# Optimization experiments

Measured on AMD Instinct MI355X. Metric: run time of the kernel, lower is better.

Reference implementation:

```python
import jax, jax.numpy as jnp
import numpy as np

Q, T, N = 1024, 256, 100
EPS = 1e-6


def setup_inputs() -> dict:
    key = jax.random.key(0)
    ks = jax.random.split(key, 8)
    return {
        'pred_curve_points': jax.random.normal(ks[0], (1, Q, N, 3), jnp.float32),
        'pred_curve_logits': jax.random.normal(ks[1], (1, Q, 2), jnp.float32),
        'pred_curve_type': jax.random.normal(ks[2], (1, Q, 4), jnp.float32),
        'closed_curve_logits': jax.random.normal(ks[3], (1, Q, 2), jnp.float32),
        'tgt_curve_points': jax.random.normal(ks[4], (T, N, 3), jnp.float32),
        'tgt_labels': jax.random.randint(ks[5], (T,), 0, 4, jnp.int64),
        'tgt_is_closed': jax.random.randint(ks[6], (T,), 0, 2, jnp.int64),
        'curve_length_weighting': jax.random.uniform(ks[7], (T,), jnp.float32),
    }


def reference(pred_curve_points, pred_curve_logits, pred_curve_type,
              closed_curve_logits, tgt_curve_points, tgt_labels,
              tgt_is_closed, curve_length_weighting):
    preds = pred_curve_points[0]                       # [Q,N,3] (batch_size=1)
    q, n, _ = preds.shape
    t = tgt_curve_points.shape[0]

    type_prob = jax.nn.softmax(pred_curve_type[0], axis=-1)      # [Q,4]
    valid_prob = jax.nn.softmax(pred_curve_logits[0], axis=-1)   # [Q,2]
    closed_prob = jax.nn.softmax(closed_curve_logits[0], axis=-1)  # [Q,2]

    # classification cost [Q,T]
    cost_class = (-jnp.log(type_prob[:, tgt_labels] + EPS)
                  - jnp.log(valid_prob[:, 0:1] + EPS)
                  - jnp.log(closed_prob[:, tgt_is_closed] + EPS))

    # cyclic variants of each target curve: all rolls of fwd + reversed orders
    j = jnp.arange(n)
    R = (j[None, :] - j[:, None]) % n                  # R[k, j] = (j-k) % n
    v_fwd = tgt_curve_points[:, R, :]                  # [T,N,N,3]
    v_bwd = tgt_curve_points[:, ::-1, :][:, R, :]      # [T,N,N,3]
    variants = jnp.concatenate([v_fwd, v_bwd], axis=1).reshape(t, 2 * n, 3 * n)
    preds_flat = preds.reshape(q, 3 * n)

    # squared cdist on flattened curves / n  (|a|^2 + |b|^2 - 2 a.b)
    ab = jnp.einsum('tvd,qd->tvq', variants, preds_flat)
    v2 = jnp.sum(tgt_curve_points ** 2, axis=(1, 2))[:, None, None]
    p2 = jnp.sum(preds_flat ** 2, axis=1)[None, None, :]
    d2 = jnp.maximum(v2 + p2 - 2.0 * ab, 0.0) / n      # [T,2N,Q]

    # closed curves: min over all 2N cyclic variants, remap reversed ids
    closed_d = d2.min(axis=1)                          # [T,Q]
    closed_ids = jnp.argmin(d2, axis=1)
    closed_ids = jnp.where(closed_ids > n - 1, 2 * n - 1 - closed_ids, closed_ids)
    # open curves: min over identity (variant 0) and full reversal (variant N)
    open_d = jnp.minimum(d2[:, 0], d2[:, n])           # [T,Q]

    is_closed_b = (tgt_is_closed > 0)[:, None]
    geom = jnp.where(is_closed_b, closed_d, open_d).T  # [Q,T]
    ids = jnp.where(is_closed_b, closed_ids, 0).T.astype(jnp.int32)

    geom = geom * curve_length_weighting[None, :]
    C = 1.0 * geom + 1.0 * cost_class                  # cost_position=cost_class=1
    return C, ids
```

## Files before the change

### kernel.cpp

```cpp
#include <hip/hip_runtime.h>
#include <hip/hip_fp16.h>

#define Q_TOT 1024
#define T_TOT 256
#define NPTS  100
#define KD    300
#define EPSV  1e-6f

#define KSTEPS 10
#define EXTOFF 40
#define EXTLEN 672

typedef _Float16 f16;
typedef _Float16 f16x8 __attribute__((ext_vector_type(8)));
typedef float    f32x4 __attribute__((ext_vector_type(4)));
#define MFMA16 __builtin_amdgcn_mfma_f32_16x16x32_f16

#define WS_PF 1280

__global__ __launch_bounds__(256) void prep_all(const float* __restrict__ preds,
                                                const float* __restrict__ tgt,
                                                float* __restrict__ ws)
{
    __shared__ __align__(16) float ext[16][308];
    const int b   = blockIdx.x;
    const int tid = threadIdx.x;

    {
        const float4* src = (const float4*)(preds + b*16*KD);
        for (int i = tid; i < 1200; i += 256) {
            int row = i / 75;
            int c   = i - row*75;
            *(float4*)&ext[row][c*4] = src[i];
        }
    }
    __syncthreads();

    f16x8* pf = (f16x8*)(ws + WS_PF) + b*1280;
    for (int j = tid; j < 1280; j += 256) {
        int lane = j & 63;
        int r    = j >> 6;
        int s    = r & 1;
        int ks   = r >> 1;
        int qr   = lane & 15;
        int kb   = ks*32 + (lane >> 4)*8;
        f16x8 v;
        #pragma unroll
        for (int jj = 0; jj < 8; ++jj) {
            int k = kb + jj;
            float x = (k < KD) ? ext[qr][k] : 0.f;
            f16 h = (f16)x;
            v[jj] = s ? (f16)(x - (float)h) : h;
        }
        pf[j] = v;
    }

    const int wv   = tid >> 6;
    const int lane = tid & 63;
    #pragma unroll
    for (int rr = 0; rr < 4; ++rr) {
        int row = wv*4 + rr;
        float s = 0.f;
        for (int k = lane; k < KD; k += 64) s = fmaf(ext[row][k], ext[row][k], s);
        #pragma unroll
        for (int m = 1; m < 64; m <<= 1) s += __shfl_xor(s, m, 64);
        if (lane == 0) ws[b*16 + row] = s;
    }
    {
        const float* base = tgt + (b*4 + wv)*KD;
        float s = 0.f;
        for (int k = lane; k < KD; k += 64) s = fmaf(base[k], base[k], s);
        #pragma unroll
        for (int m = 1; m < 64; m <<= 1) s += __shfl_xor(s, m, 64);
        if (lane == 0) ws[1024 + b*4 + wv] = s;
    }
}

template<int SEL, int VOFF>
__device__ __forceinline__ void sweep2(const f16 (*sext)[8][EXTLEN],
                                       const f16x8* __restrict__ pfrag,
                                       int ntg0, int lane, int col, int rg, int cA,
                                       float v2t, const float (&p2v)[2],
                                       float (&minD)[2], int (&minI)[2],
                                       float (*sopen)[256], int ntl0)
{
    f32x4 acc[7][2];
    #pragma unroll
    for (int h = 0; h < 7; ++h)
        #pragma unroll
        for (int nt = 0; nt < 2; ++nt) acc[h][nt] = (f32x4){0.f,0.f,0.f,0.f};

    #pragma clang loop unroll(disable)
    for (int ks = 0; ks < KSTEPS; ++ks) {
        f16x8 bh[2], bl[2];
        #pragma unroll
        for (int nt = 0; nt < 2; ++nt) {
            const int fi = ((ntg0+nt)*KSTEPS + ks)*128 + lane;
            bh[nt] = pfrag[fi];
            bl[nt] = pfrag[fi + 64];
        }
        {
            f16x8 ah[7];
            #pragma unroll
            for (int h = 0; h < 7; ++h) {
                const int idx = EXTOFF + 300 - 48*h - 3*col + 8*rg - cA + 32*ks;
                ah[h] = *(const f16x8*)&sext[SEL][cA][idx];
            }
            #pragma unroll
            for (int nt = 0; nt < 2; ++nt)
                #pragma unroll
                for (int h = 0; h < 7; ++h)
                    acc[h][nt] = MFMA16(ah[h], bh[nt], acc[h][nt], 0,0,0);
            #pragma unroll
            for (int nt = 0; nt < 2; ++nt)
                #pragma unroll
                for (int h = 0; h < 7; ++h)
                    acc[h][nt] = MFMA16(ah[h], bl[nt], acc[h][nt], 0,0,0);
        }
        {
            f16x8 alo[7];
            #pragma unroll
            for (int h = 0; h < 7; ++h) {
                const int idx = EXTOFF + 300 - 48*h - 3*col + 8*rg - cA + 32*ks;
                alo[h] = *(const f16x8*)&sext[SEL+1][cA][idx];
            }
            #pragma unroll
            for (int nt = 0; nt < 2; ++nt)
                #pragma unroll
                for (int h = 0; h < 7; ++h)
                    acc[h][nt] = MFMA16(alo[h], bh[nt], acc[h][nt], 0,0,0);
        }
    }

    #pragma unroll
    for (int h = 0; h < 7; ++h) {
        const int ab = h*16 + rg*4;
        #pragma unroll
        for (int nt = 0; nt < 2; ++nt) {
            const float s2 = v2t + p2v[nt];
            #pragma unroll
            for (int r = 0; r < 4; ++r) {
                const int al = ab + r;
                if (al < 100) {
                    float d2 = fmaxf(fmaf(-2.f, acc[h][nt][r], s2), 0.f) * 0.01f;
                    int vlog = VOFF + al;
                    if (d2 < minD[nt]) { minD[nt] = d2; minI[nt] = vlog; }
                    if (al == 0) sopen[VOFF ? 1 : 0][(ntl0+nt)*16 + col] = d2;
                }
            }
        }
    }
}

__global__ __launch_bounds__(512) void matcher_mfma(
    const float* __restrict__ ws,
    const float* __restrict__ tgt,
    const float* __restrict__ plog,
    const float* __restrict__ ptyp,
    const float* __restrict__ clog,
    const int*   __restrict__ labels,
    const int*   __restrict__ iscl,
    const float* __restrict__ clw,
    float* __restrict__ out)
{
    __shared__ __align__(16) f16 sext[4][8][EXTLEN];
    __shared__ float redD[1024];
    __shared__ int   redI[1024];
    __shared__ float sopen[2][256];

    const int t    = blockIdx.x;
    const int nb   = blockIdx.y;
    const int tid  = threadIdx.x;
    const int lane = tid & 63;
    const int w    = tid >> 6;
    const int col  = lane & 15;
    const int rg   = lane >> 4;
    const int ntl0 = w*2;
    const int ntg0 = nb*16 + ntl0;

    const float* tg = tgt + t*KD;
    for (int x = tid; x < EXTLEN; x += 512) {
        int e = x - EXTOFF;
        float vF = 0.f, vR = 0.f;
        if (e >= 0 && e < 600) {
            int m = (e >= 300) ? e - 300 : e;
            vF = tg[m];
            int jj = m / 3, c3 = m - 3*jj;
            vR = tg[(NPTS-1-jj)*3 + c3];
        }
        f16 fh = (f16)vF, fl = (f16)(vF - (float)fh);
        f16 rh = (f16)vR, rl = (f16)(vR - (float)rh);
        #pragma unroll
        for (int c = 0; c < 8; ++c) {
            int y = x - c;
            if (y >= 0) {
                sext[0][c][y] = fh; sext[1][c][y] = fl;
                sext[2][c][y] = rh; sext[3][c][y] = rl;
            }
        }
    }

    const float v2t = ws[1024 + t];
    float p2v[2];
    #pragma unroll
    for (int nt = 0; nt < 2; ++nt) p2v[nt] = ws[(ntg0+nt)*16 + col];
    const f16x8* __restrict__ pfrag = (const f16x8*)(ws + WS_PF);
    const int cA = (EXTOFF + 300 - 3*col) & 7;
    __syncthreads();

    float minD[2]; int minI[2];
    #pragma unroll
    for (int nt = 0; nt < 2; ++nt) { minD[nt] = 3.4028235e38f; minI[nt] = 0; }

    sweep2<0,  0>(sext, pfrag, ntg0, lane, col, rg, cA, v2t, p2v, minD, minI, sopen, ntl0);
    sweep2<2,100>(sext, pfrag, ntg0, lane, col, rg, cA, v2t, p2v, minD, minI, sopen, ntl0);

    #pragma unroll
    for (int nt = 0; nt < 2; ++nt) {
        redD[(ntl0+nt)*64 + lane] = minD[nt];
        redI[(ntl0+nt)*64 + lane] = minI[nt];
    }
    __syncthreads();

    if (tid < 256) {
        const int lq   = tid;
        const int tile = lq >> 4;
        const int cc   = lq & 15;
        const int base = tile*64 + cc;
        float bd = redD[base]; int bi = redI[base];
        #pragma unroll
        for (int g = 1; g < 4; ++g) {
            float d = redD[base + g*16]; int i = redI[base + g*16];
            if (d < bd || (d == bd && i < bi)) { bd = d; bi = i; }
        }
        const int q = nb*256 + lq;
        int mapped = (bi <= NPTS-1) ? bi : (2*NPTS-1 - bi);
        float od   = fminf(sopen[0][lq], sopen[1][lq]);
        int   isc  = iscl[t];
        float geom = isc ? bd : od;
        int   ido  = isc ? mapped : 0;
        geom *= clw[t];

        float t0 = ptyp[q*4+0], t1 = ptyp[q*4+1];
        float t2 = ptyp[q*4+2], t3 = ptyp[q*4+3];
        float mx = fmaxf(fmaxf(t0,t1), fmaxf(t2,t3));
        float e0 = expf(t0-mx), e1 = expf(t1-mx), e2 = expf(t2-mx), e3 = expf(t3-mx);
        float rs = 1.0f/(e0+e1+e2+e3);
        int lab  = labels[t];
        float el = (lab == 0) ? e0 : (lab == 1) ? e1 : (lab == 2) ? e2 : e3;
        float cost = -logf(el*rs + EPSV);
        float v0 = plog[q*2+0], v1 = plog[q*2+1];
        cost += -logf(1.0f/(1.0f + expf(v1-v0)) + EPSV);
        float c0 = clog[q*2+0], c1 = clog[q*2+1];
        float pc = isc ? (1.0f/(1.0f + expf(c0-c1))) : (1.0f/(1.0f + expf(c1-c0)));
        cost += -logf(pc + EPSV);

        float C = geom + cost;
        out[q*T_TOT + t]               = C;
        out[Q_TOT*T_TOT + q*T_TOT + t] = (float)ido;
    }
}

extern "C" void kernel_launch(void* const* d_in, const int* in_sizes, int n_in,
                              void* d_out, int out_size, void* d_ws, size_t ws_size,
                              hipStream_t stream)
{
    const float* preds  = (const float*)d_in[0];
    const float* plog   = (const float*)d_in[1];
    const float* ptyp   = (const float*)d_in[2];
    const float* clog   = (const float*)d_in[3];
    const float* tgt    = (const float*)d_in[4];
    const int*   labels = (const int*)d_in[5];
    const int*   iscl   = (const int*)d_in[6];
    const float* clw    = (const float*)d_in[7];
    float* out = (float*)d_out;
    float* ws  = (float*)d_ws;

    prep_all    <<<dim3(64),       dim3(256), 0, stream>>>(preds, tgt, ws);
    matcher_mfma<<<dim3(T_TOT, 4), dim3(512), 0, stream>>>(
        ws, tgt, plog, ptyp, clog, labels, iscl, clw, out);
}
```

Baseline: 161.8 us.

## Fuse prep kernel into matcher, converting preds to split-f16 fragments inline

Removes the separate prep kernel and its workspace round trip. The matcher now computes target and prediction squared norms itself and builds the hi/lo f16 B fragments directly from fp32 preds inside each k-step. This saves one launch and the global write and read of the fragments. In exchange, every block redoes the conversion and norm work, reading fp32 rows per lane with strided access instead of coalesced pre-packed fragments. The conversion is also done twice, once per sweep.

```diff
diff --git a/kernel.cpp b/kernel.cpp
--- a/kernel.cpp
+++ b/kernel.cpp
@@ -16,70 +16,11 @@
 typedef float    f32x4 __attribute__((ext_vector_type(4)));
 #define MFMA16 __builtin_amdgcn_mfma_f32_16x16x32_f16
 
-#define WS_PF 1280
-
-__global__ __launch_bounds__(256) void prep_all(const float* __restrict__ preds,
-                                                const float* __restrict__ tgt,
-                                                float* __restrict__ ws)
-{
-    __shared__ __align__(16) float ext[16][308];
-    const int b   = blockIdx.x;
-    const int tid = threadIdx.x;
-
-    {
-        const float4* src = (const float4*)(preds + b*16*KD);
-        for (int i = tid; i < 1200; i += 256) {
-            int row = i / 75;
-            int c   = i - row*75;
-            *(float4*)&ext[row][c*4] = src[i];
-        }
-    }
-    __syncthreads();
-
-    f16x8* pf = (f16x8*)(ws + WS_PF) + b*1280;
-    for (int j = tid; j < 1280; j += 256) {
-        int lane = j & 63;
-        int r    = j >> 6;
-        int s    = r & 1;
-        int ks   = r >> 1;
-        int qr   = lane & 15;
-        int kb   = ks*32 + (lane >> 4)*8;
-        f16x8 v;
-        #pragma unroll
-        for (int jj = 0; jj < 8; ++jj) {
-            int k = kb + jj;
-            float x = (k < KD) ? ext[qr][k] : 0.f;
-            f16 h = (f16)x;
-            v[jj] = s ? (f16)(x - (float)h) : h;
-        }
-        pf[j] = v;
-    }
-
-    const int wv   = tid >> 6;
-    const int lane = tid & 63;
-    #pragma unroll
-    for (int rr = 0; rr < 4; ++rr) {
-        int row = wv*4 + rr;
-        float s = 0.f;
-        for (int k = lane; k < KD; k += 64) s = fmaf(ext[row][k], ext[row][k], s);
-        #pragma unroll
-        for (int m = 1; m < 64; m <<= 1) s += __shfl_xor(s, m, 64);
-        if (lane == 0) ws[b*16 + row] = s;
-    }
-    {
-        const float* base = tgt + (b*4 + wv)*KD;
-        float s = 0.f;
-        for (int k = lane; k < KD; k += 64) s = fmaf(base[k], base[k], s);
-        #pragma unroll
-        for (int m = 1; m < 64; m <<= 1) s += __shfl_xor(s, m, 64);
-        if (lane == 0) ws[1024 + b*4 + wv] = s;
-    }
-}
-
 template<int SEL, int VOFF>
 __device__ __forceinline__ void sweep2(const f16 (*sext)[8][EXTLEN],
-                                       const f16x8* __restrict__ pfrag,
-                                       int ntg0, int lane, int col, int rg, int cA,
+                                       const float* __restrict__ prow0,
+                                       const float* __restrict__ prow1,
+                                       int lane, int col, int rg, int cA,
                                        float v2t, const float (&p2v)[2],
                                        float (&minD)[2], int (&minI)[2],
                                        float (*sopen)[256], int ntl0)
@@ -92,12 +33,29 @@
 
     #pragma clang loop unroll(disable)
     for (int ks = 0; ks < KSTEPS; ++ks) {
+        const int k0 = ks*32 + rg*8;
+        float x0[8], x1[8];
+        if (ks != KSTEPS-1) {
+            float4 a0 = *(const float4*)(prow0 + k0);
+            float4 a1 = *(const float4*)(prow0 + k0 + 4);
+            x0[0]=a0.x; x0[1]=a0.y; x0[2]=a0.z; x0[3]=a0.w;
+            x0[4]=a1.x; x0[5]=a1.y; x0[6]=a1.z; x0[7]=a1.w;
+            float4 b0 = *(const float4*)(prow1 + k0);
+            float4 b1 = *(const float4*)(prow1 + k0 + 4);
+            x1[0]=b0.x; x1[1]=b0.y; x1[2]=b0.z; x1[3]=b0.w;
+            x1[4]=b1.x; x1[5]=b1.y; x1[6]=b1.z; x1[7]=b1.w;
+        } else {
+            #pragma unroll
+            for (int j = 0; j < 8; ++j) {
+                x0[j] = (k0+j < KD) ? prow0[k0+j] : 0.f;
+                x1[j] = (k0+j < KD) ? prow1[k0+j] : 0.f;
+            }
+        }
         f16x8 bh[2], bl[2];
         #pragma unroll
-        for (int nt = 0; nt < 2; ++nt) {
-            const int fi = ((ntg0+nt)*KSTEPS + ks)*128 + lane;
-            bh[nt] = pfrag[fi];
-            bl[nt] = pfrag[fi + 64];
+        for (int j = 0; j < 8; ++j) {
+            f16 h0 = (f16)x0[j]; bh[0][j] = h0; bl[0][j] = (f16)(x0[j] - (float)h0);
+            f16 h1 = (f16)x1[j]; bh[1][j] = h1; bl[1][j] = (f16)(x1[j] - (float)h1);
         }
         {
             f16x8 ah[7];
@@ -152,8 +110,8 @@
     }
 }
 
-__global__ __launch_bounds__(512) void matcher_mfma(
-    const float* __restrict__ ws,
+__global__ __launch_bounds__(512) void matcher_fused(
+    const float* __restrict__ preds,
     const float* __restrict__ tgt,
     const float* __restrict__ plog,
     const float* __restrict__ ptyp,
@@ -200,11 +158,31 @@
         }
     }
 
-    const float v2t = ws[1024 + t];
+    float v2t;
+    {
+        float s = 0.f;
+        for (int k = lane; k < KD; k += 64) s = fmaf(tg[k], tg[k], s);
+        #pragma unroll
+        for (int m = 1; m < 64; m <<= 1) s += __shfl_xor(s, m, 64);
+        v2t = s;
+    }
+
     float p2v[2];
-    #pragma unroll
-    for (int nt = 0; nt < 2; ++nt) p2v[nt] = ws[(ntg0+nt)*16 + col];
-    const f16x8* __restrict__ pfrag = (const f16x8*)(ws + WS_PF);
+    {
+        const int qbase = ntg0*16;
+        const float4* pr = (const float4*)(preds + (qbase + (lane & 31))*KD);
+        float s = 0.f;
+        #pragma clang loop unroll(disable)
+        for (int i = 0; i < 75; ++i) {
+            float4 v = pr[i];
+            s = fmaf(v.x,v.x, fmaf(v.y,v.y, fmaf(v.z,v.z, fmaf(v.w,v.w, s))));
+        }
+        p2v[0] = __shfl(s, col,      64);
+        p2v[1] = __shfl(s, 16 + col, 64);
+    }
+
+    const float* prow0 = preds + ((ntg0+0)*16 + col)*KD;
+    const float* prow1 = preds + ((ntg0+1)*16 + col)*KD;
     const int cA = (EXTOFF + 300 - 3*col) & 7;
     __syncthreads();
 
@@ -212,8 +190,8 @@
     #pragma unroll
     for (int nt = 0; nt < 2; ++nt) { minD[nt] = 3.4028235e38f; minI[nt] = 0; }
 
-    sweep2<0,  0>(sext, pfrag, ntg0, lane, col, rg, cA, v2t, p2v, minD, minI, sopen, ntl0);
-    sweep2<2,100>(sext, pfrag, ntg0, lane, col, rg, cA, v2t, p2v, minD, minI, sopen, ntl0);
+    sweep2<0,  0>(sext, prow0, prow1, lane, col, rg, cA, v2t, p2v, minD, minI, sopen, ntl0);
+    sweep2<2,100>(sext, prow0, prow1, lane, col, rg, cA, v2t, p2v, minD, minI, sopen, ntl0);
 
     #pragma unroll
     for (int nt = 0; nt < 2; ++nt) {
@@ -274,9 +252,8 @@
     const int*   iscl   = (const int*)d_in[6];
     const float* clw    = (const float*)d_in[7];
     float* out = (float*)d_out;
-    float* ws  = (float*)d_ws;
-
-    prep_all    <<<dim3(64),       dim3(256), 0, stream>>>(preds, tgt, ws);
-    matcher_mfma<<<dim3(T_TOT, 4), dim3(512), 0, stream>>>(
-        ws, tgt, plog, ptyp, clog, labels, iscl, clw, out);
+    (void)d_ws; (void)ws_size;
+
+    matcher_fused<<<dim3(T_TOT, 4), dim3(512), 0, stream>>>(
+        preds, tgt, plog, ptyp, clog, labels, iscl, clw, out);
 }
```

Measured after the change: 253.6 us. 56.7% more time.
